# Optimization experiments

Measured on AMD Instinct MI355X. Metric: run time of the kernel, lower is better.

## Reference

```python
import jax, jax.numpy as jnp
import numpy as np
import math

BS, S, DIM, H = 2, 2048, 1024, 16
DH = DIM // H


def setup_inputs() -> dict:
    key = jax.random.key(0)
    ks = jax.random.split(key, 11)
    std = 1.0 / math.sqrt(DIM)
    inp = {
        "query": jax.random.normal(ks[0], (BS, S, DIM), jnp.float32),
        "key_": jax.random.normal(ks[1], (BS, S, DIM), jnp.float32),
        "value": jax.random.normal(ks[2], (BS, S, DIM), jnp.float32),
        "mask": jnp.ones((BS, S), jnp.int32),
        "q_w": jax.random.normal(ks[3], (DIM, DIM), jnp.float32) * std,
        "q_b": jnp.zeros((DIM,), jnp.float32),
        "k_w": jax.random.normal(ks[4], (DIM, DIM), jnp.float32) * std,
        "k_b": jnp.zeros((DIM,), jnp.float32),
        "v_w": jax.random.normal(ks[5], (DIM, DIM), jnp.float32) * std,
        "v_b": jnp.zeros((DIM,), jnp.float32),
        "o_w": jax.random.normal(ks[6], (DIM, DIM), jnp.float32) * std,
        "o_b": jnp.zeros((DIM,), jnp.float32),
    }
    return inp


def _shape(x):
    # (bs, s, dim) -> (bs, h, s, dh)
    return x.reshape(BS, -1, H, DH).transpose(0, 2, 1, 3)


def reference(query, key_, value, mask, q_w, q_b, k_w, k_b, v_w, v_b, o_w, o_b):
    # linear projections (torch Linear: x @ W.T + b)
    q = _shape(query @ q_w.T + q_b) / math.sqrt(DH)
    k = _shape(key_ @ k_w.T + k_b)
    v = _shape(value @ v_w.T + v_b)
    # scores: (bs, h, s, s)
    scores = jnp.einsum("bhqd,bhkd->bhqk", q, k)
    pad = (mask == 0)[:, None, None, :]  # (bs,1,1,k_len)
    scores = jnp.where(pad, -jnp.inf, scores)
    weights = jax.nn.softmax(scores, axis=-1)
    context = jnp.einsum("bhqk,bhkd->bhqd", weights, v)
    context = context.transpose(0, 2, 1, 3).reshape(BS, -1, DIM)
    return context @ o_w.T + o_b
```

## Files before the change

kernel.cpp:

```cpp
#include <hip/hip_runtime.h>
#include <hip/hip_bf16.h>

#define BSZ 2
#define SEQ 2048
#define DIMN 1024
#define NH 16
#define DH 64
#define LOG2E 1.4426950408889634f

typedef unsigned short ushort_t;
typedef __attribute__((ext_vector_type(8))) short short8;
typedef __attribute__((ext_vector_type(4))) float float4v;

__device__ __forceinline__ ushort_t f2bf(float f) {
    union { float f; unsigned int u; } c; c.f = f;
    return (ushort_t)((c.u + 0x8000u) >> 16);
}
__device__ __forceinline__ unsigned int pkbf(float a, float b) {
    __hip_bfloat162 h = __float22bfloat162_rn(make_float2(a, b));
    unsigned int u; __builtin_memcpy(&u, &h, 4); return u;
}
__device__ __forceinline__ unsigned int pkbf_asm(float a, float b) {
    unsigned int d;
    asm("v_cvt_pk_bf16_f32 %0, %1, %2" : "=v"(d) : "v"(a), "v"(b));
    return d;
}
__device__ __forceinline__ float exp2_raw(float x) {
    float d; asm("v_exp_f32 %0, %1" : "=v"(d) : "v"(x)); return d;
}
__device__ __forceinline__ float max3f(float a, float b, float c) {
    float d; asm("v_max3_f32 %0, %1, %2, %3" : "=v"(d) : "v"(a), "v"(b), "v"(c)); return d;
}
__device__ __forceinline__ void gld16(const ushort_t* g, ushort_t* l) {
    __builtin_amdgcn_global_load_lds(
        (const __attribute__((address_space(1))) unsigned int*)g,
        (__attribute__((address_space(3))) unsigned int*)l, 16, 0, 0);
}

__global__ __launch_bounds__(256) void cvt_all(
    const float* __restrict__ w0, const float* __restrict__ w1,
    const float* __restrict__ w2, const float* __restrict__ w3,
    const float* __restrict__ x0, const float* __restrict__ x1,
    const float* __restrict__ x2,
    ushort_t* __restrict__ o0, ushort_t* __restrict__ o1,
    ushort_t* __restrict__ o2, ushort_t* __restrict__ o3,
    ushort_t* __restrict__ xb)
{
    const int y = blockIdx.y;
    if (y < 4) {
        const float* s; ushort_t* d;
        switch (y) {
            case 0: s = w0; d = o0; break;
            case 1: s = w1; d = o1; break;
            case 2: s = w2; d = o2; break;
            default: s = w3; d = o3; break;
        }
        int i = (blockIdx.x * 256 + threadIdx.x) * 4;
        float4v v = *(const float4v*)(s + i);
        uint2 o; o.x = pkbf(v[0], v[1]); o.y = pkbf(v[2], v[3]);
        *(uint2*)(d + i) = o;
    } else {
        const int m = y - 4;
        const float* s = (m == 0) ? x0 : (m == 1) ? x1 : x2;
        ushort_t* d = xb + (size_t)m * (BSZ * SEQ * DIMN);
        size_t base = (size_t)blockIdx.x * 4096;
#pragma unroll
        for (int j = 0; j < 4; ++j) {
            size_t i = base + j * 1024 + threadIdx.x * 4;
            float4v v = *(const float4v*)(s + i);
            uint2 o; o.x = pkbf(v[0], v[1]); o.y = pkbf(v[2], v[3]);
            *(uint2*)(d + i) = o;
        }
    }
}

__global__ __launch_bounds__(256) void gemm_qkv(
    const float* __restrict__ xq, const float* __restrict__ xk, const float* __restrict__ xv,
    const ushort_t* __restrict__ Wq, const ushort_t* __restrict__ Wk, const ushort_t* __restrict__ Wv,
    const float* __restrict__ qb, const float* __restrict__ kb, const float* __restrict__ vb,
    ushort_t* __restrict__ Qp, ushort_t* __restrict__ Kp, ushort_t* __restrict__ VpT)
{
    __shared__ ushort_t As[128 * 72];
    __shared__ ushort_t Bs[128 * 72];
    const int tid  = threadIdx.x;
    const int lane = tid & 63;
    const int w    = tid >> 6;
    const int wm   = w >> 1, wn = w & 1;
    const int quad = lane >> 4;
    const int l16  = lane & 15;
    const int mBase = blockIdx.y * 128;
    const int nGlob = blockIdx.x * 128;
    const int z     = nGlob >> 10;
    const int nBase = nGlob & 1023;
    const float*    A    = (z == 0) ? xq : (z == 1) ? xk : xv;
    const ushort_t* W    = (z == 0) ? Wq : (z == 1) ? Wk : Wv;
    const float*    bias = (z == 0) ? qb : (z == 1) ? kb : vb;

    float4v acc[4][4];
    const float4v z4 = {0.f, 0.f, 0.f, 0.f};
#pragma unroll
    for (int i = 0; i < 4; ++i)
#pragma unroll
        for (int j = 0; j < 4; ++j) acc[i][j] = z4;

    for (int k0 = 0; k0 < 1024; k0 += 64) {
        float4v a[4][2];
        short8  wb[4];
#pragma unroll
        for (int it = 0; it < 4; ++it) {
            int c = it * 256 + tid, row = c >> 3, col = (c & 7) * 8;
            const float* g = A + (size_t)(mBase + row) * 1024 + k0 + col;
            a[it][0] = *(const float4v*)g;
            a[it][1] = *(const float4v*)(g + 4);
            wb[it] = *(const short8*)(W + (size_t)(nBase + row) * 1024 + k0 + col);
        }
        __syncthreads();
#pragma unroll
        for (int it = 0; it < 4; ++it) {
            int c = it * 256 + tid, row = c >> 3, col = (c & 7) * 8;
            uint4 ua;
            ua.x = pkbf(a[it][0][0], a[it][0][1]); ua.y = pkbf(a[it][0][2], a[it][0][3]);
            ua.z = pkbf(a[it][1][0], a[it][1][1]); ua.w = pkbf(a[it][1][2], a[it][1][3]);
            *(uint4*)&As[row * 72 + col] = ua;
            *(short8*)&Bs[row * 72 + col] = wb[it];
        }
        __syncthreads();

#pragma unroll
        for (int ksub = 0; ksub < 2; ++ksub) {
            short8 af[4], bf[4];
#pragma unroll
            for (int mt = 0; mt < 4; ++mt)
                af[mt] = *(const short8*)&As[(wm * 64 + mt * 16 + l16) * 72 + ksub * 32 + quad * 8];
#pragma unroll
            for (int nt = 0; nt < 4; ++nt)
                bf[nt] = *(const short8*)&Bs[(wn * 64 + nt * 16 + l16) * 72 + ksub * 32 + quad * 8];
#pragma unroll
            for (int mt = 0; mt < 4; ++mt)
#pragma unroll
                for (int nt = 0; nt < 4; ++nt)
                    acc[mt][nt] = __builtin_amdgcn_mfma_f32_16x16x32_bf16(af[mt], bf[nt], acc[mt][nt], 0, 0, 0);
        }
    }

    const float scale = (z == 0) ? 0.125f * LOG2E : 1.0f;
    if (z < 2) {
        ushort_t* C = (z == 0) ? Qp : Kp;
#pragma unroll
        for (int mt = 0; mt < 4; ++mt)
#pragma unroll
            for (int nt = 0; nt < 4; ++nt) {
                int colg = nBase + wn * 64 + nt * 16 + l16;
                float bv = bias[colg];
#pragma unroll
                for (int r = 0; r < 4; ++r) {
                    int rowg = mBase + wm * 64 + mt * 16 + quad * 4 + r;
                    C[(size_t)rowg * 1024 + colg] = f2bf((acc[mt][nt][r] + bv) * scale);
                }
            }
    } else {
#pragma unroll
        for (int mt = 0; mt < 4; ++mt)
#pragma unroll
            for (int nt = 0; nt < 4; ++nt) {
                int n = nBase + wn * 64 + nt * 16 + l16;
                int hh = n >> 6, d = n & 63;
                float bv = bias[n];
                int rowg = mBase + wm * 64 + mt * 16 + quad * 4;
                int b = rowg >> 11, s = rowg & 2047;
                uint2 pk;
                pk.x = pkbf(acc[mt][nt][0] + bv, acc[mt][nt][1] + bv);
                pk.y = pkbf(acc[mt][nt][2] + bv, acc[mt][nt][3] + bv);
                *(uint2*)&VpT[(((size_t)(b * 16 + hh) * 64 + d) << 11) + s] = pk;
            }
    }
}

__global__ __launch_bounds__(256) void gemm_qkv_fast(
    const ushort_t* __restrict__ Xb,
    const ushort_t* __restrict__ Wq, const ushort_t* __restrict__ Wk, const ushort_t* __restrict__ Wv,
    const float* __restrict__ qb, const float* __restrict__ kb, const float* __restrict__ vb,
    ushort_t* __restrict__ Qp, ushort_t* __restrict__ Kp, ushort_t* __restrict__ VpT)
{
    __shared__ __align__(16) ushort_t As[128 * 64];
    __shared__ __align__(16) ushort_t Bs[128 * 64];
    const int tid  = threadIdx.x;
    const int lane = tid & 63;
    const int w    = tid >> 6;
    const int wm   = w >> 1, wn = w & 1;
    const int quad = lane >> 4;
    const int l16  = lane & 15;
    const int sw   = l16 & 7;
    const int mBase = blockIdx.y * 128;
    const int nGlob = blockIdx.x * 128;
    const int z     = nGlob >> 10;
    const int nBase = nGlob & 1023;
    const ushort_t* A    = Xb + (size_t)z * (BSZ * SEQ * DIMN);
    const ushort_t* W    = (z == 0) ? Wq : (z == 1) ? Wk : Wv;
    const float*    bias = (z == 0) ? qb : (z == 1) ? kb : vb;

    const int srow = tid >> 3;
    const int sc   = tid & 7;

    float4v acc[4][4];
    const float4v z4 = {0.f, 0.f, 0.f, 0.f};
#pragma unroll
    for (int i = 0; i < 4; ++i)
#pragma unroll
        for (int j = 0; j < 4; ++j) acc[i][j] = z4;

    for (int k0 = 0; k0 < 1024; k0 += 64) {
#pragma unroll
        for (int itq = 0; itq < 4; ++itq) {
            int row = itq * 32 + srow;
            int colsw = (sc ^ (row & 7)) * 8;
            gld16(A + (size_t)(mBase + row) * 1024 + k0 + colsw, &As[(itq * 32 + w * 8) * 64]);
            gld16(W + (size_t)(nBase + row) * 1024 + k0 + colsw, &Bs[(itq * 32 + w * 8) * 64]);
        }
        __syncthreads();

#pragma unroll
        for (int ksub = 0; ksub < 2; ++ksub) {
            short8 af[4], bf[4];
#pragma unroll
            for (int mt = 0; mt < 4; ++mt)
                af[mt] = *(const short8*)&As[(wm * 64 + mt * 16 + l16) * 64 + ((ksub * 4 + quad) ^ sw) * 8];
#pragma unroll
            for (int nt = 0; nt < 4; ++nt)
                bf[nt] = *(const short8*)&Bs[(wn * 64 + nt * 16 + l16) * 64 + ((ksub * 4 + quad) ^ sw) * 8];
#pragma unroll
            for (int mt = 0; mt < 4; ++mt)
#pragma unroll
                for (int nt = 0; nt < 4; ++nt)
                    acc[mt][nt] = __builtin_amdgcn_mfma_f32_16x16x32_bf16(af[mt], bf[nt], acc[mt][nt], 0, 0, 0);
        }
        __syncthreads();
    }

    const float scale = (z == 0) ? 0.125f * LOG2E : 1.0f;
    if (z < 2) {
        ushort_t* C = (z == 0) ? Qp : Kp;
#pragma unroll
        for (int mt = 0; mt < 4; ++mt)
#pragma unroll
            for (int nt = 0; nt < 4; ++nt) {
                int colg = nBase + wn * 64 + nt * 16 + l16;
                float bv = bias[colg];
#pragma unroll
                for (int r = 0; r < 4; ++r) {
                    int rowg = mBase + wm * 64 + mt * 16 + quad * 4 + r;
                    C[(size_t)rowg * 1024 + colg] = f2bf((acc[mt][nt][r] + bv) * scale);
                }
            }
    } else {
#pragma unroll
        for (int mt = 0; mt < 4; ++mt)
#pragma unroll
            for (int nt = 0; nt < 4; ++nt) {
                int n = nBase + wn * 64 + nt * 16 + l16;
                int hh = n >> 6, d = n & 63;
                float bv = bias[n];
                int rowg = mBase + wm * 64 + mt * 16 + quad * 4;
                int b = rowg >> 11, s = rowg & 2047;
                uint2 pk;
                pk.x = pkbf(acc[mt][nt][0] + bv, acc[mt][nt][1] + bv);
                pk.y = pkbf(acc[mt][nt][2] + bv, acc[mt][nt][3] + bv);
                *(uint2*)&VpT[(((size_t)(b * 16 + hh) * 64 + d) << 11) + s] = pk;
            }
    }
}

__global__ __launch_bounds__(256) void gemm_o(
    const ushort_t* __restrict__ A, const ushort_t* __restrict__ W,
    const float* __restrict__ bias, float* __restrict__ C)
{
    __shared__ __align__(16) ushort_t As[128 * 64];
    __shared__ __align__(16) ushort_t Bs[64 * 64];
    const int tid  = threadIdx.x;
    const int lane = tid & 63;
    const int w    = tid >> 6;
    const int wm   = w & 1, wn = w >> 1;
    const int quad = lane >> 4;
    const int l16  = lane & 15;
    const int sw   = l16 & 7;
    const int mBase = blockIdx.y * 128;
    const int nBase = blockIdx.x * 64;
    const int srow = tid >> 3;
    const int sc   = tid & 7;

    float4v acc[4][2];
    const float4v z4 = {0.f, 0.f, 0.f, 0.f};
#pragma unroll
    for (int mt = 0; mt < 4; ++mt)
#pragma unroll
        for (int nt = 0; nt < 2; ++nt) acc[mt][nt] = z4;

    for (int k0 = 0; k0 < 1024; k0 += 64) {
#pragma unroll
        for (int itq = 0; itq < 4; ++itq) {
            int row = itq * 32 + srow;
            gld16(A + (size_t)(mBase + row) * 1024 + k0 + ((sc ^ (row & 7)) * 8),
                  &As[(itq * 32 + w * 8) * 64]);
        }
#pragma unroll
        for (int itq = 0; itq < 2; ++itq) {
            int row = itq * 32 + srow;
            gld16(W + (size_t)(nBase + row) * 1024 + k0 + ((sc ^ (row & 7)) * 8),
                  &Bs[(itq * 32 + w * 8) * 64]);
        }
        __syncthreads();

#pragma unroll
        for (int ksub = 0; ksub < 2; ++ksub) {
            short8 af[4], bf[2];
#pragma unroll
            for (int mt = 0; mt < 4; ++mt)
                af[mt] = *(const short8*)&As[(wm * 64 + mt * 16 + l16) * 64 + ((ksub * 4 + quad) ^ sw) * 8];
#pragma unroll
            for (int nt = 0; nt < 2; ++nt)
                bf[nt] = *(const short8*)&Bs[(wn * 32 + nt * 16 + l16) * 64 + ((ksub * 4 + quad) ^ sw) * 8];
#pragma unroll
            for (int mt = 0; mt < 4; ++mt)
#pragma unroll
                for (int nt = 0; nt < 2; ++nt)
                    acc[mt][nt] = __builtin_amdgcn_mfma_f32_16x16x32_bf16(af[mt], bf[nt], acc[mt][nt], 0, 0, 0);
        }
        __syncthreads();
    }

#pragma unroll
    for (int mt = 0; mt < 4; ++mt)
#pragma unroll
        for (int nt = 0; nt < 2; ++nt) {
            int colg = nBase + wn * 32 + nt * 16 + l16;
            float bv = bias[colg];
#pragma unroll
            for (int r = 0; r < 4; ++r) {
                int rowg = mBase + wm * 64 + mt * 16 + quad * 4 + r;
                C[(size_t)rowg * 1024 + colg] = acc[mt][nt][r] + bv;
            }
        }
}

__global__ __launch_bounds__(512) void attn_kernel(
    const ushort_t* __restrict__ Qp, const ushort_t* __restrict__ Kp,
    const ushort_t* __restrict__ VpT, const int* __restrict__ mask,
    ushort_t* __restrict__ Cp)
{
    __shared__ __align__(16) ushort_t Ps[2][128 * 64];
    __shared__ __align__(16) ushort_t Ks[2][64 * 64];
    __shared__ __align__(16) ushort_t Vt[3][64 * 64];
    __shared__ int s_mok[8];

    const int tid  = threadIdx.x;
    const int lane = tid & 63;
    const int w    = tid >> 6;
    const int quad = lane >> 4;
    const int l16  = lane & 15;
    const int sw   = l16 & 7;
    const int b    = blockIdx.x >> 4;
    const int h    = blockIdx.x & 15;
    const int q0   = blockIdx.y * 128;

    const int srow = tid >> 3;
    const int sc   = tid & 7;
    const int gsc  = (sc ^ (srow & 7)) * 8;
    const ushort_t* Vbase = VpT + ((size_t)(b * 16 + h) * 64) * 2048;
    const ushort_t* Kbase = Kp + (size_t)b * SEQ * DIMN + h * DH;
    const ushort_t* Qbase = Qp + (size_t)(b * SEQ + q0) * DIMN + h * DH;

    {
        int m0 = mask[b * SEQ + tid];
        int m1 = mask[b * SEQ + 512 + tid];
        int m2 = mask[b * SEQ + 1024 + tid];
        int m3 = mask[b * SEQ + 1536 + tid];
        int ok = __all((m0 != 0) & (m1 != 0) & (m2 != 0) & (m3 != 0));
        if (lane == 0) s_mok[w] = ok;
    }

#pragma unroll
    for (int it2 = 0; it2 < 2; ++it2) {
        int row = it2 * 64 + srow;
        gld16(Qbase + (size_t)row * DIMN + ((sc ^ (row & 7)) * 8),
              &Ps[0][(it2 * 64 + w * 8) * 64]);
    }
    gld16(Kbase + (size_t)srow * DIMN + gsc, &Ks[0][w * 512]);
    gld16(Vbase + (size_t)srow * 2048 + gsc, &Vt[0][w * 512]);
    __syncthreads();

    const int mall = s_mok[0] & s_mok[1] & s_mok[2] & s_mok[3]
                   & s_mok[4] & s_mok[5] & s_mok[6] & s_mok[7];

    short8 bq[2];
#pragma unroll
    for (int ks = 0; ks < 2; ++ks)
        bq[ks] = *(const short8*)&Ps[0][(w * 16 + l16) * 64 + ((4 * ks + quad) ^ sw) * 8];

    const float4v z4 = {0.f, 0.f, 0.f, 0.f};
    float4v Oacc[4];
#pragma unroll
    for (int vt = 0; vt < 4; ++vt) Oacc[vt] = z4;
    float4v Lacc = z4;
    float mrow = 0.0f;
    float4v mneg4 = z4;

    short8 ones;
#pragma unroll
    for (int j = 0; j < 8; ++j) ones[j] = (short)0x3F80;

    const int NT = SEQ / 64;
    const int prow = (w * 16 + l16) * 64;

    {
        gld16(Kbase + (size_t)(64 + srow) * DIMN + gsc, &Ks[1][w * 512]);
        gld16(Vbase + (size_t)srow * 2048 + 64 + gsc, &Vt[1][w * 512]);

        float4v Sv[4];
        __builtin_amdgcn_s_setprio(1);
#pragma unroll
        for (int kt = 0; kt < 4; ++kt) {
            short8 ak = *(const short8*)&Ks[0][(kt * 16 + l16) * 64 + (quad ^ sw) * 8];
            Sv[kt] = __builtin_amdgcn_mfma_f32_16x16x32_bf16(ak, bq[0], mneg4, 0, 0, 0);
        }
#pragma unroll
        for (int kt = 0; kt < 4; ++kt) {
            short8 ak = *(const short8*)&Ks[0][(kt * 16 + l16) * 64 + ((4 + quad) ^ sw) * 8];
            Sv[kt] = __builtin_amdgcn_mfma_f32_16x16x32_bf16(ak, bq[1], Sv[kt], 0, 0, 0);
        }
        __builtin_amdgcn_s_setprio(0);

        if (!mall) {
#pragma unroll
            for (int kt = 0; kt < 4; ++kt) {
                int4 mv = *(const int4*)(mask + b * SEQ + kt * 16 + quad * 4);
#pragma unroll
                for (int r = 0; r < 4; ++r) {
                    int m = (r == 0) ? mv.x : (r == 1) ? mv.y : (r == 2) ? mv.z : mv.w;
                    Sv[kt][r] += (m == 0) ? -1e30f : 0.0f;
                }
            }
        }

        float a0 = max3f(Sv[0][0], Sv[0][1], Sv[0][2]);
        float a1 = max3f(Sv[0][3], Sv[1][0], Sv[1][1]);
        float a2 = max3f(Sv[1][2], Sv[1][3], Sv[2][0]);
        float a3 = max3f(Sv[2][1], Sv[2][2], Sv[2][3]);
        float a4 = max3f(Sv[3][0], Sv[3][1], Sv[3][2]);
        float b0 = max3f(a0, a1, Sv[3][3]);
        float b1 = max3f(a2, a3, a4);
        float mx = fmaxf(b0, b1);
        mx = fmaxf(mx, __shfl_xor(mx, 16));
        mx = fmaxf(mx, __shfl_xor(mx, 32));
        if (!__all(mx <= 8.0f)) {
            float d = fmaxf(mx, 0.0f);
            float alpha = exp2_raw(-d);
            mrow += d;
#pragma unroll
            for (int vt = 0; vt < 4; ++vt) Oacc[vt] *= alpha;
            Lacc *= alpha;
#pragma unroll
            for (int kt = 0; kt < 4; ++kt)
#pragma unroll
                for (int r = 0; r < 4; ++r) Sv[kt][r] -= d;
            mneg4[0] = -mrow; mneg4[1] = -mrow; mneg4[2] = -mrow; mneg4[3] = -mrow;
        }
#pragma unroll
        for (int kt = 0; kt < 4; ++kt)
#pragma unroll
            for (int r = 0; r < 4; ++r) Sv[kt][r] = exp2_raw(Sv[kt][r]);

#pragma unroll
        for (int kt = 0; kt < 4; ++kt) {
            uint2 pk;
            pk.x = pkbf_asm(Sv[kt][0], Sv[kt][1]);
            pk.y = pkbf_asm(Sv[kt][2], Sv[kt][3]);
            int chunk = (2 * kt + (quad >> 1)) ^ sw;
            *(uint2*)&Ps[0][prow + chunk * 8 + (quad & 1) * 4] = pk;
        }
        __syncthreads();
    }

    ushort_t* vRd  = Vt[0];
    ushort_t* vCur = Vt[1];
    ushort_t* vWr  = Vt[2];

#pragma unroll 2
    for (int t = 1; t < NT; ++t) {
        const int kt0 = t * 64;

        if (t + 1 < NT) {
            gld16(Kbase + (size_t)(kt0 + 64 + srow) * DIMN + gsc, &Ks[(t + 1) & 1][w * 512]);
            gld16(Vbase + (size_t)srow * 2048 + kt0 + 64 + gsc, vWr + w * 512);
        }

        float4v Sv[4];
        __builtin_amdgcn_s_setprio(1);
#pragma unroll
        for (int kt = 0; kt < 4; ++kt) {
            short8 ak = *(const short8*)&Ks[t & 1][(kt * 16 + l16) * 64 + (quad ^ sw) * 8];
            Sv[kt] = __builtin_amdgcn_mfma_f32_16x16x32_bf16(ak, bq[0], mneg4, 0, 0, 0);
        }
#pragma unroll
        for (int kt = 0; kt < 4; ++kt) {
            short8 ak = *(const short8*)&Ks[t & 1][(kt * 16 + l16) * 64 + ((4 + quad) ^ sw) * 8];
            Sv[kt] = __builtin_amdgcn_mfma_f32_16x16x32_bf16(ak, bq[1], Sv[kt], 0, 0, 0);
        }
#pragma unroll
        for (int ks = 0; ks < 2; ++ks) {
            short8 bp = *(const short8*)&Ps[(t - 1) & 1][prow + ((4 * ks + quad) ^ sw) * 8];
            Lacc = __builtin_amdgcn_mfma_f32_16x16x32_bf16(ones, bp, Lacc, 0, 0, 0);
#pragma unroll
            for (int vt = 0; vt < 4; ++vt) {
                short8 av = *(const short8*)(vRd + (vt * 16 + l16) * 64 + ((4 * ks + quad) ^ sw) * 8);
                Oacc[vt] = __builtin_amdgcn_mfma_f32_16x16x32_bf16(av, bp, Oacc[vt], 0, 0, 0);
            }
        }
        __builtin_amdgcn_s_setprio(0);

        if (!mall) {
#pragma unroll
            for (int kt = 0; kt < 4; ++kt) {
                int4 mv = *(const int4*)(mask + b * SEQ + kt0 + kt * 16 + quad * 4);
#pragma unroll
                for (int r = 0; r < 4; ++r) {
                    int m = (r == 0) ? mv.x : (r == 1) ? mv.y : (r == 2) ? mv.z : mv.w;
                    Sv[kt][r] += (m == 0) ? -1e30f : 0.0f;
                }
            }
        }

        float a0 = max3f(Sv[0][0], Sv[0][1], Sv[0][2]);
        float a1 = max3f(Sv[0][3], Sv[1][0], Sv[1][1]);
        float a2 = max3f(Sv[1][2], Sv[1][3], Sv[2][0]);
        float a3 = max3f(Sv[2][1], Sv[2][2], Sv[2][3]);
        float a4 = max3f(Sv[3][0], Sv[3][1], Sv[3][2]);
        float b0 = max3f(a0, a1, Sv[3][3]);
        float b1 = max3f(a2, a3, a4);
        float mx = fmaxf(b0, b1);
        mx = fmaxf(mx, __shfl_xor(mx, 16));
        mx = fmaxf(mx, __shfl_xor(mx, 32));
        if (!__all(mx <= 8.0f)) {
            float d = fmaxf(mx, 0.0f);
            float alpha = exp2_raw(-d);
            mrow += d;
#pragma unroll
            for (int vt = 0; vt < 4; ++vt) Oacc[vt] *= alpha;
            Lacc *= alpha;
#pragma unroll
            for (int kt = 0; kt < 4; ++kt)
#pragma unroll
                for (int r = 0; r < 4; ++r) Sv[kt][r] -= d;
            mneg4[0] = -mrow; mneg4[1] = -mrow; mneg4[2] = -mrow; mneg4[3] = -mrow;
        }
#pragma unroll
        for (int kt = 0; kt < 4; ++kt)
#pragma unroll
            for (int r = 0; r < 4; ++r) Sv[kt][r] = exp2_raw(Sv[kt][r]);

#pragma unroll
        for (int kt = 0; kt < 4; ++kt) {
            uint2 pk;
            pk.x = pkbf_asm(Sv[kt][0], Sv[kt][1]);
            pk.y = pkbf_asm(Sv[kt][2], Sv[kt][3]);
            int chunk = (2 * kt + (quad >> 1)) ^ sw;
            *(uint2*)&Ps[t & 1][prow + chunk * 8 + (quad & 1) * 4] = pk;
        }

        __syncthreads();

        ushort_t* tmp = vRd; vRd = vCur; vCur = vWr; vWr = tmp;
    }

#pragma unroll
    for (int ks = 0; ks < 2; ++ks) {
        short8 bp = *(const short8*)&Ps[(NT - 1) & 1][prow + ((4 * ks + quad) ^ sw) * 8];
        Lacc = __builtin_amdgcn_mfma_f32_16x16x32_bf16(ones, bp, Lacc, 0, 0, 0);
#pragma unroll
        for (int vt = 0; vt < 4; ++vt) {
            short8 av = *(const short8*)(vRd + (vt * 16 + l16) * 64 + ((4 * ks + quad) ^ sw) * 8);
            Oacc[vt] = __builtin_amdgcn_mfma_f32_16x16x32_bf16(av, bp, Oacc[vt], 0, 0, 0);
        }
    }

    float inv = 1.0f / Lacc[0];
    int row = q0 + w * 16 + l16;
#pragma unroll
    for (int vt = 0; vt < 4; ++vt) {
        uint2 pk;
        pk.x = pkbf_asm(Oacc[vt][0] * inv, Oacc[vt][1] * inv);
        pk.y = pkbf_asm(Oacc[vt][2] * inv, Oacc[vt][3] * inv);
        *(uint2*)&Cp[(size_t)(b * SEQ + row) * DIMN + h * DH + vt * 16 + quad * 4] = pk;
    }
}

extern "C" void kernel_launch(void* const* d_in, const int* in_sizes, int n_in,
                              void* d_out, int out_size, void* d_ws, size_t ws_size,
                              hipStream_t stream) {
    const float* x_q = (const float*)d_in[0];
    const float* x_k = (const float*)d_in[1];
    const float* x_v = (const float*)d_in[2];
    const int*   msk = (const int*)d_in[3];
    const float* q_w = (const float*)d_in[4];
    const float* q_b = (const float*)d_in[5];
    const float* k_w = (const float*)d_in[6];
    const float* k_b = (const float*)d_in[7];
    const float* v_w = (const float*)d_in[8];
    const float* v_b = (const float*)d_in[9];
    const float* o_w = (const float*)d_in[10];
    const float* o_b = (const float*)d_in[11];
    float* out = (float*)d_out;

    const size_t NEL = (size_t)BSZ * SEQ * DIMN;
    const size_t WEL = (size_t)DIMN * DIMN;
    ushort_t* Qp  = (ushort_t*)d_ws;
    ushort_t* Kp  = Qp + NEL;
    ushort_t* VpT = Kp + NEL;
    ushort_t* Wq  = VpT + NEL;
    ushort_t* Wk  = Wq + WEL;
    ushort_t* Wv  = Wk + WEL;
    ushort_t* Wo  = Wv + WEL;
    ushort_t* Xb  = Wo + WEL;
    ushort_t* Cp  = Qp;

    const bool fast = ws_size >= ((size_t)56 << 20);
    if (fast) {
        cvt_all<<<dim3(1024, 7), 256, 0, stream>>>(q_w, k_w, v_w, o_w, x_q, x_k, x_v,
                                                   Wq, Wk, Wv, Wo, Xb);
        gemm_qkv_fast<<<dim3(24, 32), 256, 0, stream>>>(Xb, Wq, Wk, Wv,
                                                        q_b, k_b, v_b, Qp, Kp, VpT);
    } else {
        cvt_all<<<dim3(1024, 4), 256, 0, stream>>>(q_w, k_w, v_w, o_w, x_q, x_k, x_v,
                                                   Wq, Wk, Wv, Wo, Xb);
        gemm_qkv<<<dim3(24, 32), 256, 0, stream>>>(x_q, x_k, x_v, Wq, Wk, Wv,
                                                   q_b, k_b, v_b, Qp, Kp, VpT);
    }
    attn_kernel<<<dim3(BSZ * NH, SEQ / 128), 512, 0, stream>>>(Qp, Kp, VpT, msk, Cp);
    gemm_o<<<dim3(16, 32), 256, 0, stream>>>(Cp, Wo, o_b, out);
}
```

Baseline: 225.3 us.

## Fuse activation fp32-to-bf16 conversion into QKV GEMM, drop separate conversion pass

Removes the separate pass that converts the three fp32 input activations to bf16 in a workspace buffer. The QKV GEMM now loads fp32 activations directly, converts them in registers and writes them into the swizzled shared-memory tile, while weights still use async global-to-LDS loads. This avoids a full write and re-read of a 3x8MB-equivalent bf16 intermediate, at the cost of the GEMM doing synchronous register-path loads for A. It also removes the workspace-size branch.

```diff
diff --git a/kernel.cpp b/kernel.cpp
--- a/kernel.cpp
+++ b/kernel.cpp
@@ -37,147 +37,27 @@
         (__attribute__((address_space(3))) unsigned int*)l, 16, 0, 0);
 }
 
-__global__ __launch_bounds__(256) void cvt_all(
+__global__ __launch_bounds__(256) void cvt_w4(
     const float* __restrict__ w0, const float* __restrict__ w1,
     const float* __restrict__ w2, const float* __restrict__ w3,
-    const float* __restrict__ x0, const float* __restrict__ x1,
-    const float* __restrict__ x2,
     ushort_t* __restrict__ o0, ushort_t* __restrict__ o1,
-    ushort_t* __restrict__ o2, ushort_t* __restrict__ o3,
-    ushort_t* __restrict__ xb)
+    ushort_t* __restrict__ o2, ushort_t* __restrict__ o3)
 {
-    const int y = blockIdx.y;
-    if (y < 4) {
-        const float* s; ushort_t* d;
-        switch (y) {
-            case 0: s = w0; d = o0; break;
-            case 1: s = w1; d = o1; break;
-            case 2: s = w2; d = o2; break;
-            default: s = w3; d = o3; break;
-        }
-        int i = (blockIdx.x * 256 + threadIdx.x) * 4;
-        float4v v = *(const float4v*)(s + i);
-        uint2 o; o.x = pkbf(v[0], v[1]); o.y = pkbf(v[2], v[3]);
-        *(uint2*)(d + i) = o;
-    } else {
-        const int m = y - 4;
-        const float* s = (m == 0) ? x0 : (m == 1) ? x1 : x2;
-        ushort_t* d = xb + (size_t)m * (BSZ * SEQ * DIMN);
-        size_t base = (size_t)blockIdx.x * 4096;
-#pragma unroll
-        for (int j = 0; j < 4; ++j) {
-            size_t i = base + j * 1024 + threadIdx.x * 4;
-            float4v v = *(const float4v*)(s + i);
-            uint2 o; o.x = pkbf(v[0], v[1]); o.y = pkbf(v[2], v[3]);
-            *(uint2*)(d + i) = o;
-        }
-    }
-}
-
-__global__ __launch_bounds__(256) void gemm_qkv(
+    const float* s; ushort_t* d;
+    switch (blockIdx.y) {
+        case 0: s = w0; d = o0; break;
+        case 1: s = w1; d = o1; break;
+        case 2: s = w2; d = o2; break;
+        default: s = w3; d = o3; break;
+    }
+    int i = (blockIdx.x * 256 + threadIdx.x) * 4;
+    float4v v = *(const float4v*)(s + i);
+    uint2 o; o.x = pkbf(v[0], v[1]); o.y = pkbf(v[2], v[3]);
+    *(uint2*)(d + i) = o;
+}
+
+__global__ __launch_bounds__(256) void gemm_qkv_hyb(
     const float* __restrict__ xq, const float* __restrict__ xk, const float* __restrict__ xv,
-    const ushort_t* __restrict__ Wq, const ushort_t* __restrict__ Wk, const ushort_t* __restrict__ Wv,
-    const float* __restrict__ qb, const float* __restrict__ kb, const float* __restrict__ vb,
-    ushort_t* __restrict__ Qp, ushort_t* __restrict__ Kp, ushort_t* __restrict__ VpT)
-{
-    __shared__ ushort_t As[128 * 72];
-    __shared__ ushort_t Bs[128 * 72];
-    const int tid  = threadIdx.x;
-    const int lane = tid & 63;
-    const int w    = tid >> 6;
-    const int wm   = w >> 1, wn = w & 1;
-    const int quad = lane >> 4;
-    const int l16  = lane & 15;
-    const int mBase = blockIdx.y * 128;
-    const int nGlob = blockIdx.x * 128;
-    const int z     = nGlob >> 10;
-    const int nBase = nGlob & 1023;
-    const float*    A    = (z == 0) ? xq : (z == 1) ? xk : xv;
-    const ushort_t* W    = (z == 0) ? Wq : (z == 1) ? Wk : Wv;
-    const float*    bias = (z == 0) ? qb : (z == 1) ? kb : vb;
-
-    float4v acc[4][4];
-    const float4v z4 = {0.f, 0.f, 0.f, 0.f};
-#pragma unroll
-    for (int i = 0; i < 4; ++i)
-#pragma unroll
-        for (int j = 0; j < 4; ++j) acc[i][j] = z4;
-
-    for (int k0 = 0; k0 < 1024; k0 += 64) {
-        float4v a[4][2];
-        short8  wb[4];
-#pragma unroll
-        for (int it = 0; it < 4; ++it) {
-            int c = it * 256 + tid, row = c >> 3, col = (c & 7) * 8;
-            const float* g = A + (size_t)(mBase + row) * 1024 + k0 + col;
-            a[it][0] = *(const float4v*)g;
-            a[it][1] = *(const float4v*)(g + 4);
-            wb[it] = *(const short8*)(W + (size_t)(nBase + row) * 1024 + k0 + col);
-        }
-        __syncthreads();
-#pragma unroll
-        for (int it = 0; it < 4; ++it) {
-            int c = it * 256 + tid, row = c >> 3, col = (c & 7) * 8;
-            uint4 ua;
-            ua.x = pkbf(a[it][0][0], a[it][0][1]); ua.y = pkbf(a[it][0][2], a[it][0][3]);
-            ua.z = pkbf(a[it][1][0], a[it][1][1]); ua.w = pkbf(a[it][1][2], a[it][1][3]);
-            *(uint4*)&As[row * 72 + col] = ua;
-            *(short8*)&Bs[row * 72 + col] = wb[it];
-        }
-        __syncthreads();
-
-#pragma unroll
-        for (int ksub = 0; ksub < 2; ++ksub) {
-            short8 af[4], bf[4];
-#pragma unroll
-            for (int mt = 0; mt < 4; ++mt)
-                af[mt] = *(const short8*)&As[(wm * 64 + mt * 16 + l16) * 72 + ksub * 32 + quad * 8];
-#pragma unroll
-            for (int nt = 0; nt < 4; ++nt)
-                bf[nt] = *(const short8*)&Bs[(wn * 64 + nt * 16 + l16) * 72 + ksub * 32 + quad * 8];
-#pragma unroll
-            for (int mt = 0; mt < 4; ++mt)
-#pragma unroll
-                for (int nt = 0; nt < 4; ++nt)
-                    acc[mt][nt] = __builtin_amdgcn_mfma_f32_16x16x32_bf16(af[mt], bf[nt], acc[mt][nt], 0, 0, 0);
-        }
-    }
-
-    const float scale = (z == 0) ? 0.125f * LOG2E : 1.0f;
-    if (z < 2) {
-        ushort_t* C = (z == 0) ? Qp : Kp;
-#pragma unroll
-        for (int mt = 0; mt < 4; ++mt)
-#pragma unroll
-            for (int nt = 0; nt < 4; ++nt) {
-                int colg = nBase + wn * 64 + nt * 16 + l16;
-                float bv = bias[colg];
-#pragma unroll
-                for (int r = 0; r < 4; ++r) {
-                    int rowg = mBase + wm * 64 + mt * 16 + quad * 4 + r;
-                    C[(size_t)rowg * 1024 + colg] = f2bf((acc[mt][nt][r] + bv) * scale);
-                }
-            }
-    } else {
-#pragma unroll
-        for (int mt = 0; mt < 4; ++mt)
-#pragma unroll
-            for (int nt = 0; nt < 4; ++nt) {
-                int n = nBase + wn * 64 + nt * 16 + l16;
-                int hh = n >> 6, d = n & 63;
-                float bv = bias[n];
-                int rowg = mBase + wm * 64 + mt * 16 + quad * 4;
-                int b = rowg >> 11, s = rowg & 2047;
-                uint2 pk;
-                pk.x = pkbf(acc[mt][nt][0] + bv, acc[mt][nt][1] + bv);
-                pk.y = pkbf(acc[mt][nt][2] + bv, acc[mt][nt][3] + bv);
-                *(uint2*)&VpT[(((size_t)(b * 16 + hh) * 64 + d) << 11) + s] = pk;
-            }
-    }
-}
-
-__global__ __launch_bounds__(256) void gemm_qkv_fast(
-    const ushort_t* __restrict__ Xb,
     const ushort_t* __restrict__ Wq, const ushort_t* __restrict__ Wk, const ushort_t* __restrict__ Wv,
     const float* __restrict__ qb, const float* __restrict__ kb, const float* __restrict__ vb,
     ushort_t* __restrict__ Qp, ushort_t* __restrict__ Kp, ushort_t* __restrict__ VpT)
@@ -195,7 +75,7 @@
     const int nGlob = blockIdx.x * 128;
     const int z     = nGlob >> 10;
     const int nBase = nGlob & 1023;
-    const ushort_t* A    = Xb + (size_t)z * (BSZ * SEQ * DIMN);
+    const float*    A    = (z == 0) ? xq : (z == 1) ? xk : xv;
     const ushort_t* W    = (z == 0) ? Wq : (z == 1) ? Wk : Wv;
     const float*    bias = (z == 0) ? qb : (z == 1) ? kb : vb;
 
@@ -214,8 +94,18 @@
         for (int itq = 0; itq < 4; ++itq) {
             int row = itq * 32 + srow;
             int colsw = (sc ^ (row & 7)) * 8;
-            gld16(A + (size_t)(mBase + row) * 1024 + k0 + colsw, &As[(itq * 32 + w * 8) * 64]);
             gld16(W + (size_t)(nBase + row) * 1024 + k0 + colsw, &Bs[(itq * 32 + w * 8) * 64]);
+        }
+#pragma unroll
+        for (int it = 0; it < 4; ++it) {
+            int c = it * 256 + tid, row = c >> 3, col8 = c & 7;
+            const float* g = A + (size_t)(mBase + row) * 1024 + k0 + col8 * 8;
+            float4v a0 = *(const float4v*)g;
+            float4v a1 = *(const float4v*)(g + 4);
+            uint4 ua;
+            ua.x = pkbf(a0[0], a0[1]); ua.y = pkbf(a0[2], a0[3]);
+            ua.z = pkbf(a1[0], a1[1]); ua.w = pkbf(a1[2], a1[3]);
+            *(uint4*)&As[row * 64 + ((col8 ^ (row & 7)) * 8)] = ua;
         }
         __syncthreads();
 
@@ -619,21 +509,11 @@
     ushort_t* Wk  = Wq + WEL;
     ushort_t* Wv  = Wk + WEL;
     ushort_t* Wo  = Wv + WEL;
-    ushort_t* Xb  = Wo + WEL;
     ushort_t* Cp  = Qp;
 
-    const bool fast = ws_size >= ((size_t)56 << 20);
-    if (fast) {
-        cvt_all<<<dim3(1024, 7), 256, 0, stream>>>(q_w, k_w, v_w, o_w, x_q, x_k, x_v,
-                                                   Wq, Wk, Wv, Wo, Xb);
-        gemm_qkv_fast<<<dim3(24, 32), 256, 0, stream>>>(Xb, Wq, Wk, Wv,
-                                                        q_b, k_b, v_b, Qp, Kp, VpT);
-    } else {
-        cvt_all<<<dim3(1024, 4), 256, 0, stream>>>(q_w, k_w, v_w, o_w, x_q, x_k, x_v,
-                                                   Wq, Wk, Wv, Wo, Xb);
-        gemm_qkv<<<dim3(24, 32), 256, 0, stream>>>(x_q, x_k, x_v, Wq, Wk, Wv,
+    cvt_w4<<<dim3(WEL / 1024, 4), 256, 0, stream>>>(q_w, k_w, v_w, o_w, Wq, Wk, Wv, Wo);
+    gemm_qkv_hyb<<<dim3(24, 32), 256, 0, stream>>>(x_q, x_k, x_v, Wq, Wk, Wv,
                                                    q_b, k_b, v_b, Qp, Kp, VpT);
-    }
     attn_kernel<<<dim3(BSZ * NH, SEQ / 128), 512, 0, stream>>>(Qp, Kp, VpT, msk, Cp);
     gemm_o<<<dim3(16, 32), 256, 0, stream>>>(Cp, Wo, o_b, out);
 }
```

Result: slower. 240.8 us (+6.9%).
